# Kernel optimization log

Hardware: AMD Instinct MI355X
Metric: run time of the kernel (lower is better)

## Reference

```python
import jax, jax.numpy as jnp
import numpy as np

# ---- geometry constants (from init_kwargs) ----
VOL_SHAPE = (96, 96, 96)        # (Z, Y, X)
VOL_SPACING = 1.0               # mm, isotropic
N_PROJ = 180
DET_ROWS, DET_COLS = 192, 384   # (v, u)
DET_SPACING_V, DET_SPACING_U = 1.0, 1.0
SID = 750.0                     # source-isocenter distance
SDD = 1200.0                    # source-detector distance


def _proj_matrices():
    """3x4 pinhole projection matrices for a circular cone-beam trajectory."""
    cu = (DET_COLS - 1) / 2.0
    cv = (DET_ROWS - 1) / 2.0
    Kc = np.array([[SDD / DET_SPACING_U, 0.0, cu],
                   [0.0, SDD / DET_SPACING_V, cv],
                   [0.0, 0.0, 1.0]])
    mats = []
    for th in np.linspace(0.0, 2.0 * np.pi, N_PROJ, endpoint=False):
        s = SID * np.array([np.cos(th), np.sin(th), 0.0])   # source position
        ez = -s / SID                                        # optical axis -> isocenter
        ex = np.array([-np.sin(th), np.cos(th), 0.0])        # detector u axis
        ey = np.array([0.0, 0.0, 1.0])                       # detector v axis
        R = np.stack([ex, ey, ez])                           # world -> camera
        P = Kc @ np.concatenate([R, (-R @ s)[:, None]], axis=1)
        mats.append(P)
    return np.stack(mats).astype(np.float32)                # [P, 3, 4]


def _voxel_coords():
    """Homogeneous world coordinates of all voxel centers, [4, N]."""
    zs = (np.arange(VOL_SHAPE[0]) - (VOL_SHAPE[0] - 1) / 2.0) * VOL_SPACING
    ys = (np.arange(VOL_SHAPE[1]) - (VOL_SHAPE[1] - 1) / 2.0) * VOL_SPACING
    xs = (np.arange(VOL_SHAPE[2]) - (VOL_SHAPE[2] - 1) / 2.0) * VOL_SPACING
    Z, Y, X = np.meshgrid(zs, ys, xs, indexing='ij')
    pts = np.stack([X.ravel(), Y.ravel(), Z.ravel(), np.ones(X.size)])
    return pts.astype(np.float32)


def _bilinear(img, u, v):
    """Zero-padded bilinear interpolation of img[H,W] at (v,u) pixel coords."""
    H, W = img.shape
    u0 = jnp.floor(u); v0 = jnp.floor(v)
    fu = u - u0; fv = v - v0
    u0i = u0.astype(jnp.int32); v0i = v0.astype(jnp.int32)
    def at(vi, ui):
        valid = (ui >= 0) & (ui < W) & (vi >= 0) & (vi < H)
        val = img[jnp.clip(vi, 0, H - 1), jnp.clip(ui, 0, W - 1)]
        return jnp.where(valid, val, jnp.zeros((), img.dtype))
    return (at(v0i, u0i) * (1 - fu) * (1 - fv)
            + at(v0i, u0i + 1) * fu * (1 - fv)
            + at(v0i + 1, u0i) * (1 - fu) * fv
            + at(v0i + 1, u0i + 1) * fu * fv)


def _backproject_one(sino, mats, coords):
    """sino [P,H,W], mats [P,3,4], coords [4,N] -> volume [Z,Y,X]."""
    N = coords.shape[1]
    @jax.checkpoint
    def step(acc, pm_s):
        P, s = pm_s
        uvw = P @ coords                      # [3, N]
        w = uvw[2]                            # ray depth along optical axis (>0)
        u = uvw[0] / w
        v = uvw[1] / w
        acc = acc + _bilinear(s, u, v) / (w * w)  # FDK distance weighting
        return acc, None
    acc, _ = jax.lax.scan(step, jnp.zeros((N,), sino.dtype), (mats, sino))
    return acc.reshape(VOL_SHAPE)


def setup_inputs() -> dict:
    key = jax.random.key(0)
    x = jax.random.normal(key, (2, N_PROJ, DET_ROWS, DET_COLS, 1), dtype=jnp.float32)
    proj_matrices = jnp.asarray(_proj_matrices())
    return {"x": x, "proj_matrices": proj_matrices}


def reference(x, proj_matrices):
    coords = jnp.asarray(_voxel_coords())                 # [4, N]
    sinos = jnp.squeeze(x, -1)                            # [B, P, H, W]
    vols = jax.vmap(lambda s: _backproject_one(s, proj_matrices, coords))(sinos)
    return vols[..., None]                                # [B, Z, Y, X, 1]
```

## Files before the change

kernel.cpp:

```cpp
#include <hip/hip_runtime.h>

#define NPROJ 180
#define PHALF 90
#define DH 192
#define DW 384
#define VN 96
#define ZPER 4
#define TCOLS 65
#define TPAD 1024
#define PSTRIDE (DH * DW)
#define BSTRIDE (NPROJ * DH * DW)

typedef float v2f __attribute__((ext_vector_type(2)));

#define BARRIER_LDS() do {                                          \
    __builtin_amdgcn_fence(__ATOMIC_RELEASE, "workgroup", "local"); \
    __builtin_amdgcn_s_barrier();                                   \
    __builtin_amdgcn_fence(__ATOMIC_ACQUIRE, "workgroup", "local"); \
} while (0)

__global__ __launch_bounds__(256, 6) void cone_bp(
    const float* __restrict__ sino,
    const float* __restrict__ mats,
    float* __restrict__ out)
{
    __shared__ v2f tile[2][TPAD];
    __shared__ int2 anch[PHALF];

    const int tid = threadIdx.x;
    const int x = blockIdx.x * 32 + ((tid & 7) | ((tid >> 6) << 3));
    const int y = blockIdx.y * 8 + ((tid >> 3) & 7);
    const int half = (blockIdx.z >= 24) ? 1 : 0;
    const int zc = blockIdx.z - 24 * half;
    const int pbase = half * PHALF;

    const float xw = (float)x - 47.5f;
    const float yw = (float)y - 47.5f;
    const float zw0 = (float)(zc * ZPER) - 47.5f;

    const float xwc = (float)(blockIdx.x * 32) - 32.0f;
    const float ywc = (float)(blockIdx.y * 8) - 44.0f;
    const float zwc = (float)(zc * ZPER) - 46.0f;

    const float4* __restrict__ M = (const float4*)mats;

    if (tid < PHALF) {
        int p = pbase + tid;
        float4 a0 = M[p * 3 + 0];
        float4 a1 = M[p * 3 + 1];
        float4 a2 = M[p * 3 + 2];
        float unc = fmaf(a0.x, xwc, fmaf(a0.y, ywc, a0.w));
        float vnc = fmaf(a1.x, xwc, fmaf(a1.y, ywc, fmaf(a1.z, zwc, a1.w)));
        float wc  = fmaf(a2.x, xwc, fmaf(a2.y, ywc, a2.w));
        float rwc = __builtin_amdgcn_rcpf(wc);
        anch[tid] = make_int2((int)floorf(unc * rwc) - 31,
                              (int)floorf(vnc * rwc) - 6);
    }

    int VgB[4];
#pragma unroll
    for (int k = 0; k < 4; ++k) {
        int li = tid + 256 * k;
        int row = li / TCOLS;
        int col = li - row * TCOLS;
        VgB[k] = (row * DW + col) * 4;
    }

    __syncthreads();

    int cu, cv;
    {
        int2 a = anch[0];
        cu = __builtin_amdgcn_readfirstlane(a.x);
        cv = __builtin_amdgcn_readfirstlane(a.y);
    }
    v2f g[4];
    {
        const char* p0 = (const char*)(sino + pbase * PSTRIDE + cv * DW + cu);
        const char* p1 = p0 + (size_t)BSTRIDE * 4;
#pragma unroll
        for (int k = 0; k < 4; ++k) {
            g[k].x = *(const float*)(p0 + VgB[k]);
            g[k].y = *(const float*)(p1 + VgB[k]);
        }
    }

    v2f acc[ZPER];
#pragma unroll
    for (int k = 0; k < ZPER; ++k) acc[k] = (v2f)(0.0f);

    auto body = [&](int i, v2f* __restrict__ buf) {
#pragma unroll
        for (int k = 0; k < 4; ++k)
            buf[tid + 256 * k] = g[k];
        const float nfu = -(float)cu;
        const float nfv = -(float)cv;

        if (i + 1 < PHALF) {
            int2 a = anch[i + 1];
            cu = __builtin_amdgcn_readfirstlane(a.x);
            cv = __builtin_amdgcn_readfirstlane(a.y);
            const char* p0 = (const char*)(sino
                + (pbase + i + 1) * PSTRIDE + cv * DW + cu);
            const char* p1 = p0 + (size_t)BSTRIDE * 4;
#pragma unroll
            for (int k = 0; k < 4; ++k) {
                g[k].x = *(const float*)(p0 + VgB[k]);
                g[k].y = *(const float*)(p1 + VgB[k]);
            }
        }

        BARRIER_LDS();

        const int p = pbase + i;
        float4 r0 = M[p * 3 + 0];
        float4 r1 = M[p * 3 + 1];
        float4 r2 = M[p * 3 + 2];
        float un  = fmaf(r0.x, xw, fmaf(r0.y, yw, r0.w));
        float vn0 = fmaf(r1.x, xw, fmaf(r1.y, yw, r1.w));
        float w   = fmaf(r2.x, xw, fmaf(r2.y, yw, r2.w));
        float rw  = __builtin_amdgcn_rcpf(w);
        float iw2 = rw * rw;
        float ul  = fmaf(un, rw, nfu);
        float uf  = floorf(ul);
        float fu  = ul - uf;
        int   u0l = (int)uf;
        float vb  = fmaf(fmaf(r1.z, zw0, vn0), rw, nfv);
        float dv  = r1.z * rw;

        int   o[ZPER];
        float fv[ZPER];
#pragma unroll
        for (int k = 0; k < ZPER; ++k) {
            float v  = fmaf(dv, (float)k, vb);
            float vf = floorf(v);
            fv[k] = v - vf;
            o[k] = (int)vf * TCOLS + u0l;
        }
        v2f E00[ZPER], E01[ZPER], E10[ZPER], E11[ZPER];
#pragma unroll
        for (int k = 0; k < ZPER; ++k) {
            E00[k] = buf[o[k]];
            E01[k] = buf[o[k] + 1];
            E10[k] = buf[o[k] + TCOLS];
            E11[k] = buf[o[k] + TCOLS + 1];
        }
#pragma unroll
        for (int k = 0; k < ZPER; ++k) {
            v2f F0 = E00[k] + (E10[k] - E00[k]) * fv[k];
            v2f F1 = E01[k] + (E11[k] - E01[k]) * fv[k];
            v2f H  = F0 + (F1 - F0) * fu;
            acc[k] += H * iw2;
        }
    };

    for (int i = 0; i < PHALF; i += 2) {
        body(i,     tile[0]);
        body(i + 1, tile[1]);
    }

    const int zbase = zc * ZPER;
#pragma unroll
    for (int k = 0; k < ZPER; ++k) {
        unsafeAtomicAdd(&out[(((size_t)(zbase + k)) * VN + y) * VN + x],
                        acc[k].x);
        unsafeAtomicAdd(&out[(((size_t)(VN + zbase + k)) * VN + y) * VN + x],
                        acc[k].y);
    }
}

extern "C" void kernel_launch(void* const* d_in, const int* in_sizes, int n_in,
                              void* d_out, int out_size, void* d_ws, size_t ws_size,
                              hipStream_t stream) {
    const float* sino = (const float*)d_in[0];
    const float* mats = (const float*)d_in[1];
    float* out = (float*)d_out;

    hipMemsetAsync(out, 0, (size_t)out_size * sizeof(float), stream);

    dim3 grid(VN / 32, VN / 8, 48), block(256);
    hipLaunchKernelGGL(cone_bp, grid, block, 0, stream, sino, mats, out);
}
```

Measured before the change: 301.3 us.

## Split projections into quarters with workspace accumulation to increase block parallelism

Templates the backprojection kernel on projection-chunk size and splits the 180 angles into four quarters instead of two, doubling the grid. Two quarters accumulate into a zeroed workspace to spread atomic contention, and a small kernel adds the workspace into the output. Occupancy hint raised from 6 to 8 blocks per CU. Adds a memset and an extra elementwise pass plus more atomics, and tighter register limits may cause spills.

```diff
diff --git a/kernel.cpp b/kernel.cpp
--- a/kernel.cpp
+++ b/kernel.cpp
@@ -1,11 +1,11 @@
 #include <hip/hip_runtime.h>
 
 #define NPROJ 180
-#define PHALF 90
 #define DH 192
 #define DW 384
 #define VN 96
 #define ZPER 4
+#define ZCH (VN / ZPER)
 #define TCOLS 65
 #define TPAD 1024
 #define PSTRIDE (DH * DW)
@@ -19,20 +19,22 @@
     __builtin_amdgcn_fence(__ATOMIC_ACQUIRE, "workgroup", "local"); \
 } while (0)
 
-__global__ __launch_bounds__(256, 6) void cone_bp(
+template<int PQ, int NQ>
+__global__ __launch_bounds__(256, 8) void cone_bp(
     const float* __restrict__ sino,
     const float* __restrict__ mats,
-    float* __restrict__ out)
+    float* __restrict__ out,
+    float* __restrict__ ws)
 {
     __shared__ v2f tile[2][TPAD];
-    __shared__ int2 anch[PHALF];
+    __shared__ int2 anch[PQ];
 
     const int tid = threadIdx.x;
     const int x = blockIdx.x * 32 + ((tid & 7) | ((tid >> 6) << 3));
     const int y = blockIdx.y * 8 + ((tid >> 3) & 7);
-    const int half = (blockIdx.z >= 24) ? 1 : 0;
-    const int zc = blockIdx.z - 24 * half;
-    const int pbase = half * PHALF;
+    const int zc = blockIdx.z % ZCH;
+    const int qt = blockIdx.z / ZCH;
+    const int pbase = qt * PQ;
 
     const float xw = (float)x - 47.5f;
     const float yw = (float)y - 47.5f;
@@ -44,7 +46,7 @@
 
     const float4* __restrict__ M = (const float4*)mats;
 
-    if (tid < PHALF) {
+    if (tid < PQ) {
         int p = pbase + tid;
         float4 a0 = M[p * 3 + 0];
         float4 a1 = M[p * 3 + 1];
@@ -96,7 +98,7 @@
         const float nfu = -(float)cu;
         const float nfv = -(float)cv;
 
-        if (i + 1 < PHALF) {
+        if (i + 1 < PQ) {
             int2 a = anch[i + 1];
             cu = __builtin_amdgcn_readfirstlane(a.x);
             cv = __builtin_amdgcn_readfirstlane(a.y);
@@ -154,18 +156,31 @@
         }
     };
 
-    for (int i = 0; i < PHALF; i += 2) {
-        body(i,     tile[0]);
-        body(i + 1, tile[1]);
-    }
-
+    for (int i = 0; i < PQ; i += 2) {
+        body(i, tile[0]);
+        if (i + 1 < PQ) body(i + 1, tile[1]);
+    }
+
+    float* __restrict__ dst = (NQ == 4 && qt >= 2) ? ws : out;
     const int zbase = zc * ZPER;
 #pragma unroll
     for (int k = 0; k < ZPER; ++k) {
-        unsafeAtomicAdd(&out[(((size_t)(zbase + k)) * VN + y) * VN + x],
+        unsafeAtomicAdd(&dst[(((size_t)(zbase + k)) * VN + y) * VN + x],
                         acc[k].x);
-        unsafeAtomicAdd(&out[(((size_t)(VN + zbase + k)) * VN + y) * VN + x],
+        unsafeAtomicAdd(&dst[(((size_t)(VN + zbase + k)) * VN + y) * VN + x],
                         acc[k].y);
+    }
+}
+
+__global__ __launch_bounds__(256) void add_ws(
+    float4* __restrict__ out, const float4* __restrict__ ws, int n4)
+{
+    int i = blockIdx.x * 256 + threadIdx.x;
+    if (i < n4) {
+        float4 a = ws[i];
+        float4 b = out[i];
+        b.x += a.x; b.y += a.y; b.z += a.z; b.w += a.w;
+        out[i] = b;
     }
 }
 
@@ -175,9 +190,22 @@
     const float* sino = (const float*)d_in[0];
     const float* mats = (const float*)d_in[1];
     float* out = (float*)d_out;
-
+    float* wsf = (float*)d_ws;
+
+    const size_t nvox = (size_t)2 * VN * VN * VN;
     hipMemsetAsync(out, 0, (size_t)out_size * sizeof(float), stream);
 
-    dim3 grid(VN / 32, VN / 8, 48), block(256);
-    hipLaunchKernelGGL(cone_bp, grid, block, 0, stream, sino, mats, out);
+    if (ws_size >= nvox * sizeof(float)) {
+        hipMemsetAsync(wsf, 0, nvox * sizeof(float), stream);
+        dim3 grid(VN / 32, VN / 8, ZCH * 4), block(256);
+        hipLaunchKernelGGL((cone_bp<NPROJ / 4, 4>), grid, block, 0, stream,
+                           sino, mats, out, wsf);
+        int n4 = (int)(nvox / 4);
+        hipLaunchKernelGGL(add_ws, dim3((n4 + 255) / 256), block, 0, stream,
+                           (float4*)out, (const float4*)wsf, n4);
+    } else {
+        dim3 grid(VN / 32, VN / 8, ZCH * 2), block(256);
+        hipLaunchKernelGGL((cone_bp<NPROJ / 2, 2>), grid, block, 0, stream,
+                           sino, mats, out, (float*)nullptr);
+    }
 }
```

New measurement: 298.9 us. About the same (-0.8%).
